# Optimization experiments

Measured on AMD Instinct MI355X. Metric: run time of the kernel, lower is better.

Reference implementation:

```python
import jax, jax.numpy as jnp
import numpy as np

# Dimensions / config (WorldModelConfig + PredictiveLayerConfig defaults)
S, N, L = 128, 256, 3          # n_sensory, n_hidden, n_layers
T, B = 100, 512                # timesteps, batch
TAU_MEM, TAU_PRED, DT = 20.0, 50.0, 1.0
NOISE_STD, ERROR_GAIN = 0.02, 0.5
DECAY_MEM = float(np.exp(-DT / TAU_MEM))
DECAY_PRED = float(np.exp(-DT / TAU_PRED))
ALPHA = DT / TAU_PRED          # precision EMA rate


def setup_inputs() -> dict:
    key = jax.random.key(0)
    ks = jax.random.split(key, 12)
    w = lambda k, a, b, s: jax.random.normal(k, (a, b), dtype=jnp.float32) * s
    return {
        'sensory_seq': jax.random.uniform(ks[0], (T, B, S), dtype=jnp.float32),
        'ff0': w(ks[1], S, N, 0.1 / S ** 0.5),
        'ff1': w(ks[2], N, N, 0.1 / N ** 0.5),
        'ff2': w(ks[3], N, N, 0.1 / N ** 0.5),
        'rec0': w(ks[4], N, N, 0.01),
        'rec1': w(ks[5], N, N, 0.01),
        'rec2': w(ks[6], N, N, 0.01),
        'pred0': w(ks[7], N, N, 0.1 / N ** 0.5),
        'pred1': w(ks[8], N, N, 0.1 / N ** 0.5),
        'p2r0': w(ks[9], N, N, 0.1 / N ** 0.5),
        'p2r1': w(ks[10], N, N, 0.1 / N ** 0.5),
    }


def _lif(v, inp, decay, noise):
    """LIF membrane update: leak + drive + noise, threshold=1.0, reset to 0."""
    v = decay * v + inp + noise
    s = (v >= 1.0).astype(v.dtype)
    return s, v * (1.0 - s)


def reference(sensory_seq, ff0, ff1, ff2, rec0, rec1, rec2, pred0, pred1, p2r0, p2r1):
    ffs = [ff0, ff1, ff2]
    recs = [rec0, rec1, rec2]
    preds = [pred0, pred1]
    p2rs = [p2r0, p2r1]
    mask = 1.0 - jnp.eye(N, dtype=sensory_seq.dtype)   # recurrent_mask
    base_key = jax.random.key(42)
    Bsz = sensory_seq.shape[1]

    init = (
        jnp.zeros((L, Bsz, N), jnp.float32),   # repr membrane
        jnp.zeros((2, Bsz, N), jnp.float32),   # pred membrane (layers 0,1)
        jnp.zeros((L, Bsz, N), jnp.float32),   # last spikes
        jnp.ones((L, Bsz, N), jnp.float32),    # precision
    )

    def step(carry, t):
        v, pv, last, prec = carry
        nks = jax.random.split(jax.random.fold_in(base_key, t), 5)
        new_v, new_pv, new_last, new_prec, errs = [], [], [], [], []
        for i in range(L):
            # top-down prediction from layer i+1's previous-step activity
            if i < L - 1:
                pred_in = last[i + 1] @ preds[i]
                pn = (NOISE_STD * 0.5) * jax.random.normal(nks[3 + i], (Bsz, N))
                psp, pvi = _lif(pv[i], pred_in, DECAY_PRED, pn)
                prediction = psp @ p2rs[i]
                new_pv.append(pvi)
            else:
                prediction = jnp.zeros((Bsz, N), jnp.float32)
            # bottom-up input: sensory for layer 0, lower layer's current spikes above
            inp_act = sensory_seq[t] if i == 0 else new_last[i - 1]
            input_repr = inp_act @ ffs[i]
            error = input_repr - prediction
            total = prediction + error * ERROR_GAIN * prec[i] + last[i] @ (recs[i] * mask)
            noi = NOISE_STD * jax.random.normal(nks[i], (Bsz, N))
            sp, vi = _lif(v[i], total, DECAY_MEM, noi)
            # precision EMA on inverse error variance
            ev = jnp.mean(error * error, axis=1, keepdims=True) + 1e-6
            pr = (1.0 - ALPHA) * prec[i] + ALPHA * (1.0 / ev)
            new_v.append(vi); new_last.append(sp); new_prec.append(pr); errs.append(error)
        carry = (jnp.stack(new_v), jnp.stack(new_pv), jnp.stack(new_last), jnp.stack(new_prec))
        return carry, jnp.stack(errs)   # [L, B, N] per step

    _, errors = jax.lax.scan(step, init, jnp.arange(T))
    return errors   # [T, L, B, N]
```

## Files before the change

### kernel.cpp

```cpp
#include <hip/hip_runtime.h>
#include <stdint.h>

#define TSTEPS 100
#define BATCH  512
#define NH     256
#define NS     128

__device__ __forceinline__ uint32_t rotl32(uint32_t x, int r) {
  return (x << r) | (x >> (32 - r));
}

__device__ __forceinline__ void tf2x32(uint32_t k0, uint32_t k1,
                                       uint32_t c0, uint32_t c1,
                                       uint32_t& o0, uint32_t& o1) {
  const uint32_t ks2 = k0 ^ k1 ^ 0x1BD11BDAu;
  uint32_t x0 = c0 + k0, x1 = c1 + k1;
#define TFR(r) { x0 += x1; x1 = rotl32(x1, r); x1 ^= x0; }
  TFR(13) TFR(15) TFR(26) TFR(6)
  x0 += k1;  x1 += ks2 + 1u;
  TFR(17) TFR(29) TFR(16) TFR(24)
  x0 += ks2; x1 += k0 + 2u;
  TFR(13) TFR(15) TFR(26) TFR(6)
  x0 += k0;  x1 += k1 + 3u;
  TFR(17) TFR(29) TFR(16) TFR(24)
  x0 += k1;  x1 += ks2 + 4u;
  TFR(13) TFR(15) TFR(26) TFR(6)
  x0 += ks2; x1 += k0 + 5u;
#undef TFR
  o0 = x0; o1 = x1;
}

__device__ __forceinline__ float xla_vf32_log(float a) {
  uint32_t bits = __float_as_uint(a);
  float e = __fadd_rn((float)((int)(bits >> 23) - 127), 1.0f);
  float x = __uint_as_float((bits & 0x007FFFFFu) | 0x3F000000u);
  const bool mask = x < 0.707106781186547524f;
  float tmp = mask ? x : 0.0f;
  x = __fsub_rn(x, 1.0f);
  e = mask ? __fsub_rn(e, 1.0f) : e;
  x = __fadd_rn(x, tmp);
  float z = __fmul_rn(x, x);
  float y = 7.0376836292e-2f;
  y = __fmaf_rn(y, x, -1.1514610310e-1f);
  y = __fmaf_rn(y, x, 1.1676998740e-1f);
  y = __fmaf_rn(y, x, -1.2420140846e-1f);
  y = __fmaf_rn(y, x, 1.4249322787e-1f);
  y = __fmaf_rn(y, x, -1.6668057665e-1f);
  y = __fmaf_rn(y, x, 2.0000714765e-1f);
  y = __fmaf_rn(y, x, -2.4999993993e-1f);
  y = __fmaf_rn(y, x, 3.3333331174e-1f);
  y = __fmul_rn(y, x);
  y = __fmul_rn(y, z);
  y = __fmaf_rn(e, -2.12194440e-4f, y);
  y = __fmaf_rn(-0.5f, z, y);
  x = __fadd_rn(x, y);
  x = __fmaf_rn(e, 0.693359375f, x);
  return x;
}

__device__ __forceinline__ float xla_sqrt2_erfinv(float u) {
  float nxx = -__fmul_rn(u, u);
  float w;
  if (fabsf(nxx) < 1e-4f) {
    w = -__fmul_rn(__fmaf_rn(-0.5f, nxx, 1.0f), nxx);
  } else {
    w = -xla_vf32_log(__fadd_rn(nxx, 1.0f));
  }
  float p;
  if (w < 5.0f) {
    float t = __fsub_rn(w, 2.5f);
    p = 2.81022636e-08f;
    p = __fmaf_rn(p, t, 3.43273939e-07f);
    p = __fmaf_rn(p, t, -3.5233877e-06f);
    p = __fmaf_rn(p, t, -4.39150654e-06f);
    p = __fmaf_rn(p, t, 0.00021858087f);
    p = __fmaf_rn(p, t, -0.00125372503f);
    p = __fmaf_rn(p, t, -0.00417768164f);
    p = __fmaf_rn(p, t, 0.246640727f);
    p = __fmaf_rn(p, t, 1.50140941f);
  } else {
    float t = __fsub_rn(__fsqrt_rn(w), 3.0f);
    p = -0.000200214257f;
    p = __fmaf_rn(p, t, 0.000100950558f);
    p = __fmaf_rn(p, t, 0.00134934322f);
    p = __fmaf_rn(p, t, -0.00367342844f);
    p = __fmaf_rn(p, t, 0.00573950773f);
    p = __fmaf_rn(p, t, -0.0076224613f);
    p = __fmaf_rn(p, t, 0.00943887047f);
    p = __fmaf_rn(p, t, 1.00167406f);
    p = __fmaf_rn(p, t, 2.83297682f);
  }
  return __fmul_rn((float)1.4142135623730951, __fmul_rn(p, u));
}

__device__ __forceinline__ float jax_normal(uint32_t k0, uint32_t k1, uint32_t j) {
  uint32_t o0, o1;
  tf2x32(k0, k1, 0u, j, o0, o1);
  const uint32_t bits = o0 ^ o1;
  float f = __fsub_rn(__uint_as_float((bits >> 9) | 0x3f800000u), 1.0f);
  const float LO = -0.99999994f;
  float u = __fmaf_rn(f, 2.0f, LO);
  u = fmaxf(LO, u);
  return xla_sqrt2_erfinv(u);
}

__global__ void pack_w(const float* __restrict__ src, float* __restrict__ dst,
                       int K, int zero_diag) {
  int tid = blockIdx.x * 256 + threadIdx.x;
  if (tid >= K * NH) return;
  int k = tid >> 8, n = tid & 255;
  float v = src[tid];
  if (zero_diag && k == n) v = 0.f;
  dst[(((k >> 2) * NH) + n) * 4 + (k & 3)] = v;
}

__global__ __launch_bounds__(256)
void gen_noise(float* __restrict__ NZ) {
  uint32_t idx = blockIdx.x * 256u + threadIdx.x;
  uint32_t j = idx & 131071u;
  uint32_t td = idx >> 17;
  uint32_t t = td / 5u, d = td - 5u * t;
  uint32_t fk0, fk1, k0, k1;
  tf2x32(0u, 42u, 0u, t, fk0, fk1);
  tf2x32(fk0, fk1, 0u, d, k0, k1);
  float z = jax_normal(k0, k1, j);
  float scale = (d >= 3u) ? 0.01f : 0.02f;
  NZ[idx] = __fmul_rn(scale, z);
}

__device__ __forceinline__ void dot1_seg(const float4* __restrict__ P0,
                                         const float* __restrict__ A0,
                                         int n, int k4b, int k4e, float& r0) {
  float a0 = r0;
  #pragma unroll 8
  for (int k4 = k4b; k4 < k4e; ++k4) {
    float4 w0 = P0[k4 * NH + n];
    float4 x0 = *reinterpret_cast<const float4*>(A0 + 4 * k4);
    a0 = __fmaf_rn(x0.x, w0.x, a0); a0 = __fmaf_rn(x0.y, w0.y, a0);
    a0 = __fmaf_rn(x0.z, w0.z, a0); a0 = __fmaf_rn(x0.w, w0.w, a0);
  }
  r0 = a0;
}

__device__ __forceinline__ void dot2_seg(const float4* __restrict__ P0,
                                         const float* __restrict__ A0,
                                         const float4* __restrict__ P1,
                                         const float* __restrict__ A1,
                                         int n, int k4b, int k4e,
                                         float& r0, float& r1) {
  float a0 = r0, a1 = r1;
  #pragma unroll 8
  for (int k4 = k4b; k4 < k4e; ++k4) {
    float4 w0 = P0[k4 * NH + n];
    float4 w1 = P1[k4 * NH + n];
    float4 x0 = *reinterpret_cast<const float4*>(A0 + 4 * k4);
    float4 x1 = *reinterpret_cast<const float4*>(A1 + 4 * k4);
    a0 = __fmaf_rn(x0.x, w0.x, a0); a0 = __fmaf_rn(x0.y, w0.y, a0);
    a0 = __fmaf_rn(x0.z, w0.z, a0); a0 = __fmaf_rn(x0.w, w0.w, a0);
    a1 = __fmaf_rn(x1.x, w1.x, a1); a1 = __fmaf_rn(x1.y, w1.y, a1);
    a1 = __fmaf_rn(x1.z, w1.z, a1); a1 = __fmaf_rn(x1.w, w1.w, a1);
  }
  r0 = a0; r1 = a1;
}

__global__ __launch_bounds__(512)
void wm_fast5(const float* __restrict__ sensory,
              const float4* __restrict__ pred0p, const float4* __restrict__ pred1p,
              const float4* __restrict__ p2r0p,  const float4* __restrict__ rec0p,
              const float4* __restrict__ ff0p,   const float4* __restrict__ p2r1p,
              const float4* __restrict__ ff1p,   const float4* __restrict__ rec1p,
              const float4* __restrict__ ff2p,   const float4* __restrict__ rec2p,
              const float* __restrict__ NZ,
              float* __restrict__ out) {
  const int tid = threadIdx.x;
  const int n = tid & 255;
  const int h = tid >> 8;
  const int b = blockIdx.x;

  __shared__ __align__(16) float last[2][3][NH];
  __shared__ __align__(16) float psp0[NH];
  __shared__ __align__(16) float psp1[NH];
  __shared__ __align__(16) float sens[NS];
  __shared__ __align__(16) float errsq[3][NH];
  __shared__ __align__(16) float xfer[NH];
  __shared__ float evsum[3];

  if (h == 0) {
    #pragma unroll
    for (int i = 0; i < 3; ++i) { last[0][i][n] = 0.f; last[1][i][n] = 0.f; }
  }

  float pv = 0.f, vA = 0.f, vB = 0.f;
  float prec0 = 1.f, prec1 = 1.f, prec2 = 1.f;
  const float DM = (float)0.951229424500714009;
  const float DP = (float)0.980198673306755250;

  __syncthreads();

  for (int t = 0; t < TSTEPS; ++t) {
    const int p = t & 1, q = p ^ 1;
    const size_t nb = ((size_t)t * 5 * BATCH + b) * NH + n;

    if (tid < NS) sens[tid] = sensory[((size_t)t * BATCH + b) * NS + tid];
    if (h == 0) {
      float acc = 0.f;
      dot1_seg(pred0p, last[p][1], n, 0, 64, acc);
      float pn = NZ[nb + (size_t)3 * BATCH * NH];
      pv = __fadd_rn(__fmaf_rn(DP, pv, acc), pn);
      bool s = (pv >= 1.0f);
      psp0[n] = s ? 1.f : 0.f;
      pv = s ? 0.f : pv;
    } else {
      float acc = 0.f;
      dot1_seg(pred1p, last[p][2], n, 0, 64, acc);
      float pn = NZ[nb + (size_t)4 * BATCH * NH];
      pv = __fadd_rn(__fmaf_rn(DP, pv, acc), pn);
      bool s = (pv >= 1.0f);
      psp1[n] = s ? 1.f : 0.f;
      pv = s ? 0.f : pv;
    }
    __syncthreads();

    float inp_b = 0.f, rc_b = 0.f;
    if (h == 0) {
      dot2_seg(ff0p, sens, rec0p, last[p][0], n, 0, 32, inp_b, rc_b);
      dot1_seg(rec0p, last[p][0], n, 32, 64, rc_b);
    } else {
      float pr = 0.f;
      dot1_seg(p2r0p, psp0, n, 0, 64, pr);
      xfer[n] = pr;
    }
    __syncthreads();
    if (h == 0) {
      float pr = xfer[n];
      float noi = NZ[nb];
      float err = __fsub_rn(inp_b, pr);
      out[(((size_t)t * 3 + 0) * BATCH + b) * NH + n] = err;
      errsq[0][n] = __fmul_rn(err, err);
      float m1  = __fmul_rn(err, 0.5f);
      float tot = __fadd_rn(__fmaf_rn(m1, prec0, pr), rc_b);
      vA = __fadd_rn(__fmaf_rn(DM, vA, tot), noi);
      bool s = (vA >= 1.0f);
      last[q][0][n] = s ? 1.f : 0.f;
      vA = s ? 0.f : vA;
    }
    __syncthreads();

    if (h == 0) {
      float inp = 0.f;
      dot1_seg(ff1p, last[q][0], n, 0, 64, inp);
      xfer[n] = inp;
    } else {
      float pr = 0.f, rc = 0.f;
      dot2_seg(p2r1p, psp1, rec1p, last[p][1], n, 0, 64, pr, rc);
      inp_b = pr; rc_b = rc;
    }
    __syncthreads();
    if (h == 1) {
      float pr = inp_b, rc = rc_b;
      float inp = xfer[n];
      float noi = NZ[nb + (size_t)1 * BATCH * NH];
      float err = __fsub_rn(inp, pr);
      out[(((size_t)t * 3 + 1) * BATCH + b) * NH + n] = err;
      errsq[1][n] = __fmul_rn(err, err);
      float m1  = __fmul_rn(err, 0.5f);
      float tot = __fadd_rn(__fmaf_rn(m1, prec1, pr), rc);
      vA = __fadd_rn(__fmaf_rn(DM, vA, tot), noi);
      bool s = (vA >= 1.0f);
      last[q][1][n] = s ? 1.f : 0.f;
      vA = s ? 0.f : vA;
    }
    __syncthreads();

    if (h == 0) {
      float inp = 0.f;
      dot1_seg(ff2p, last[q][1], n, 0, 64, inp);
      inp_b = inp;
    } else {
      float rc = 0.f;
      dot1_seg(rec2p, last[p][2], n, 0, 64, rc);
      xfer[n] = rc;
    }
    __syncthreads();
    if (h == 0) {
      float rc = xfer[n];
      float err = inp_b;
      float noi = NZ[nb + (size_t)2 * BATCH * NH];
      out[(((size_t)t * 3 + 2) * BATCH + b) * NH + n] = err;
      errsq[2][n] = __fmul_rn(err, err);
      float m1  = __fmul_rn(err, 0.5f);
      float tot = __fadd_rn(__fmaf_rn(m1, prec2, 0.0f), rc);
      vB = __fadd_rn(__fmaf_rn(DM, vB, tot), noi);
      bool s = (vB >= 1.0f);
      last[q][2][n] = s ? 1.f : 0.f;
      vB = s ? 0.f : vB;
    }
    __syncthreads();

    if (((tid & 63) == 0) && tid < 192) {
      const float4* s4 = reinterpret_cast<const float4*>(errsq[tid >> 6]);
      float acc = 0.f;
      #pragma unroll 16
      for (int k4 = 0; k4 < 64; ++k4) {
        float4 v = s4[k4];
        acc = __fadd_rn(acc, v.x); acc = __fadd_rn(acc, v.y);
        acc = __fadd_rn(acc, v.z); acc = __fadd_rn(acc, v.w);
      }
      evsum[tid >> 6] = acc;
    }
    __syncthreads();

    {
      float ev0 = __fadd_rn(__fmul_rn(evsum[0], 0.00390625f), 1e-6f);
      float ev1 = __fadd_rn(__fmul_rn(evsum[1], 0.00390625f), 1e-6f);
      float ev2 = __fadd_rn(__fmul_rn(evsum[2], 0.00390625f), 1e-6f);
      prec0 = __fmaf_rn(0.98f, prec0, __fmul_rn(0.02f, 1.0f / ev0));
      prec1 = __fmaf_rn(0.98f, prec1, __fmul_rn(0.02f, 1.0f / ev1));
      prec2 = __fmaf_rn(0.98f, prec2, __fmul_rn(0.02f, 1.0f / ev2));
    }
  }
}

__device__ __forceinline__ float dot_lds(const float* __restrict__ a,
                                         const float* __restrict__ W,
                                         int n, int K) {
  float acc = 0.f;
  #pragma unroll 8
  for (int k = 0; k < K; ++k)
    acc = __fmaf_rn(a[k], W[k * NH + n], acc);
  return acc;
}

__device__ __forceinline__ float dot_rec(const float* __restrict__ a,
                                         const float* __restrict__ W, int n) {
  float acc = 0.f;
  #pragma unroll 8
  for (int k = 0; k < NH; ++k) {
    float w = (k == n) ? 0.f : W[k * NH + n];
    acc = __fmaf_rn(a[k], w, acc);
  }
  return acc;
}

__global__ __launch_bounds__(NH)
void wm_kernel_mono(const float* __restrict__ sensory,
                    const float* __restrict__ ff0, const float* __restrict__ ff1,
                    const float* __restrict__ ff2,
                    const float* __restrict__ rec0, const float* __restrict__ rec1,
                    const float* __restrict__ rec2,
                    const float* __restrict__ pred0, const float* __restrict__ pred1,
                    const float* __restrict__ p2r0, const float* __restrict__ p2r1,
                    float* __restrict__ out) {
  const int b = blockIdx.x;
  const int n = threadIdx.x;

  __shared__ float last[2][3][NH];
  __shared__ float psp[NH];
  __shared__ float sens[NS];
  __shared__ float errsq[3][NH];
  __shared__ float evsum[3];
  __shared__ uint32_t keys[TSTEPS][5][2];

  if (n < TSTEPS) {
    uint32_t fk0, fk1;
    tf2x32(0u, 42u, 0u, (uint32_t)n, fk0, fk1);
    #pragma unroll
    for (int i = 0; i < 5; ++i) {
      uint32_t s0, s1;
      tf2x32(fk0, fk1, 0u, (uint32_t)i, s0, s1);
      keys[n][i][0] = s0; keys[n][i][1] = s1;
    }
  }
  for (int i = 0; i < 3; ++i) { last[0][i][n] = 0.f; last[1][i][n] = 0.f; }

  float v0 = 0.f, v1 = 0.f, v2 = 0.f, pv0 = 0.f, pv1 = 0.f;
  float prec0 = 1.f, prec1 = 1.f, prec2 = 1.f;
  const float DM = (float)0.951229424500714009;
  const float DP = (float)0.980198673306755250;
  const uint32_t j = (uint32_t)(b * NH + n);

  __syncthreads();

  for (int t = 0; t < TSTEPS; ++t) {
    const int p = t & 1, q = p ^ 1;

    if (n < NS) sens[n] = sensory[((size_t)t * BATCH + b) * NS + n];
    {
      float acc = dot_lds(last[p][1], pred0, n, NH);
      float pn = __fmul_rn(0.01f, jax_normal(keys[t][3][0], keys[t][3][1], j));
      pv0 = __fadd_rn(__fmaf_rn(DP, pv0, acc), pn);
      bool s = (pv0 >= 1.0f);
      psp[n] = s ? 1.f : 0.f;
      pv0 = s ? 0.f : pv0;
    }
    __syncthreads();

    {
      float pr  = dot_lds(psp, p2r0, n, NH);
      float inp = dot_lds(sens, ff0, n, NS);
      float rc  = dot_rec(last[p][0], rec0, n);
      float err = __fsub_rn(inp, pr);
      out[(((size_t)t * 3 + 0) * BATCH + b) * NH + n] = err;
      errsq[0][n] = __fmul_rn(err, err);
      float m1  = __fmul_rn(err, 0.5f);
      float tot = __fadd_rn(__fmaf_rn(m1, prec0, pr), rc);
      float noi = __fmul_rn(0.02f, jax_normal(keys[t][0][0], keys[t][0][1], j));
      v0 = __fadd_rn(__fmaf_rn(DM, v0, tot), noi);
      bool s = (v0 >= 1.0f);
      last[q][0][n] = s ? 1.f : 0.f;
      v0 = s ? 0.f : v0;
    }
    __syncthreads();

    {
      float acc = dot_lds(last[p][2], pred1, n, NH);
      float pn = __fmul_rn(0.01f, jax_normal(keys[t][4][0], keys[t][4][1], j));
      pv1 = __fadd_rn(__fmaf_rn(DP, pv1, acc), pn);
      bool s = (pv1 >= 1.0f);
      psp[n] = s ? 1.f : 0.f;
      pv1 = s ? 0.f : pv1;
    }
    __syncthreads();

    {
      float pr  = dot_lds(psp, p2r1, n, NH);
      float inp = dot_lds(last[q][0], ff1, n, NH);
      float rc  = dot_rec(last[p][1], rec1, n);
      float err = __fsub_rn(inp, pr);
      out[(((size_t)t * 3 + 1) * BATCH + b) * NH + n] = err;
      errsq[1][n] = __fmul_rn(err, err);
      float m1  = __fmul_rn(err, 0.5f);
      float tot = __fadd_rn(__fmaf_rn(m1, prec1, pr), rc);
      float noi = __fmul_rn(0.02f, jax_normal(keys[t][1][0], keys[t][1][1], j));
      v1 = __fadd_rn(__fmaf_rn(DM, v1, tot), noi);
      bool s = (v1 >= 1.0f);
      last[q][1][n] = s ? 1.f : 0.f;
      v1 = s ? 0.f : v1;
    }
    __syncthreads();

    {
      float inp = dot_lds(last[q][1], ff2, n, NH);
      float rc  = dot_rec(last[p][2], rec2, n);
      float err = inp;
      out[(((size_t)t * 3 + 2) * BATCH + b) * NH + n] = err;
      errsq[2][n] = __fmul_rn(err, err);
      float m1  = __fmul_rn(err, 0.5f);
      float tot = __fadd_rn(__fmaf_rn(m1, prec2, 0.0f), rc);
      float noi = __fmul_rn(0.02f, jax_normal(keys[t][2][0], keys[t][2][1], j));
      v2 = __fadd_rn(__fmaf_rn(DM, v2, tot), noi);
      bool s = (v2 >= 1.0f);
      last[q][2][n] = s ? 1.f : 0.f;
      v2 = s ? 0.f : v2;
    }
    __syncthreads();

    if (((n & 63) == 0) && n < 192) {
      const float* s = errsq[n >> 6];
      float acc = 0.f;
      #pragma unroll 32
      for (int k = 0; k < NH; ++k) acc = __fadd_rn(acc, s[k]);
      evsum[n >> 6] = acc;
    }
    __syncthreads();

    {
      float ev0 = __fadd_rn(__fmul_rn(evsum[0], 0.00390625f), 1e-6f);
      float ev1 = __fadd_rn(__fmul_rn(evsum[1], 0.00390625f), 1e-6f);
      float ev2 = __fadd_rn(__fmul_rn(evsum[2], 0.00390625f), 1e-6f);
      prec0 = __fmaf_rn(0.98f, prec0, __fmul_rn(0.02f, 1.0f / ev0));
      prec1 = __fmaf_rn(0.98f, prec1, __fmul_rn(0.02f, 1.0f / ev1));
      prec2 = __fmaf_rn(0.98f, prec2, __fmul_rn(0.02f, 1.0f / ev2));
    }
  }
}

extern "C" void kernel_launch(void* const* d_in, const int* in_sizes, int n_in,
                              void* d_out, int out_size, void* d_ws, size_t ws_size,
                              hipStream_t stream) {
  (void)in_sizes; (void)n_in; (void)out_size;
  const float* sensory = (const float*)d_in[0];
  const float* ff0  = (const float*)d_in[1];
  const float* ff1  = (const float*)d_in[2];
  const float* ff2  = (const float*)d_in[3];
  const float* rec0 = (const float*)d_in[4];
  const float* rec1 = (const float*)d_in[5];
  const float* rec2 = (const float*)d_in[6];
  const float* pred0 = (const float*)d_in[7];
  const float* pred1 = (const float*)d_in[8];
  const float* p2r0 = (const float*)d_in[9];
  const float* p2r1 = (const float*)d_in[10];
  float* out = (float*)d_out;

  const size_t OFF_PRED0 = 0, OFF_PRED1 = 65536, OFF_P2R0 = 131072,
               OFF_REC0 = 196608, OFF_FF0 = 262144, OFF_P2R1 = 294912,
               OFF_FF1 = 360448, OFF_REC1 = 425984, OFF_FF2 = 491520,
               OFF_REC2 = 557056, OFF_NZ = 655360;
  const size_t NZ_FLOATS = (size_t)TSTEPS * 5 * BATCH * NH;
  const size_t NEED = (OFF_NZ + NZ_FLOATS) * sizeof(float);

  if (ws_size >= NEED) {
    float* W = (float*)d_ws;
    pack_w<<<dim3(NH * NH / 256), dim3(256), 0, stream>>>(pred0, W + OFF_PRED0, NH, 0);
    pack_w<<<dim3(NH * NH / 256), dim3(256), 0, stream>>>(pred1, W + OFF_PRED1, NH, 0);
    pack_w<<<dim3(NH * NH / 256), dim3(256), 0, stream>>>(p2r0,  W + OFF_P2R0,  NH, 0);
    pack_w<<<dim3(NH * NH / 256), dim3(256), 0, stream>>>(rec0,  W + OFF_REC0,  NH, 1);
    pack_w<<<dim3(NS * NH / 256), dim3(256), 0, stream>>>(ff0,   W + OFF_FF0,   NS, 0);
    pack_w<<<dim3(NH * NH / 256), dim3(256), 0, stream>>>(p2r1,  W + OFF_P2R1,  NH, 0);
    pack_w<<<dim3(NH * NH / 256), dim3(256), 0, stream>>>(ff1,   W + OFF_FF1,   NH, 0);
    pack_w<<<dim3(NH * NH / 256), dim3(256), 0, stream>>>(rec1,  W + OFF_REC1,  NH, 1);
    pack_w<<<dim3(NH * NH / 256), dim3(256), 0, stream>>>(ff2,   W + OFF_FF2,   NH, 0);
    pack_w<<<dim3(NH * NH / 256), dim3(256), 0, stream>>>(rec2,  W + OFF_REC2,  NH, 1);
    gen_noise<<<dim3((unsigned)(NZ_FLOATS / 256)), dim3(256), 0, stream>>>(W + OFF_NZ);
    wm_fast5<<<dim3(BATCH), dim3(512), 0, stream>>>(
        sensory,
        (const float4*)(W + OFF_PRED0), (const float4*)(W + OFF_PRED1),
        (const float4*)(W + OFF_P2R0),  (const float4*)(W + OFF_REC0),
        (const float4*)(W + OFF_FF0),   (const float4*)(W + OFF_P2R1),
        (const float4*)(W + OFF_FF1),   (const float4*)(W + OFF_REC1),
        (const float4*)(W + OFF_FF2),   (const float4*)(W + OFF_REC2),
        W + OFF_NZ, out);
  } else {
    wm_kernel_mono<<<dim3(BATCH), dim3(NH), 0, stream>>>(
        sensory, ff0, ff1, ff2, rec0, rec1, rec2,
        pred0, pred1, p2r0, p2r1, out);
  }
}
```

Measured before the change: 4.691 ms.

## Process two batch rows per block to reuse each weight load twice

Each workgroup now handles two batch rows instead of one, so every float4 weight fetched from global/L2 feeds two accumulators. Shared buffers, membrane states and precision values are all duplicated per row, and the grid is halved to 256 blocks. This targets the weight-load bandwidth of the per-step matvecs. The cost is fewer blocks than the chip has CUs, more registers per thread, and a longer serial dependency chain per block, so parallelism drops.

```diff
diff --git a/kernel.cpp b/kernel.cpp
--- a/kernel.cpp
+++ b/kernel.cpp
@@ -128,43 +128,57 @@
   NZ[idx] = __fmul_rn(scale, z);
 }
 
-__device__ __forceinline__ void dot1_seg(const float4* __restrict__ P0,
-                                         const float* __restrict__ A0,
-                                         int n, int k4b, int k4e, float& r0) {
-  float a0 = r0;
-  #pragma unroll 8
-  for (int k4 = k4b; k4 < k4e; ++k4) {
-    float4 w0 = P0[k4 * NH + n];
-    float4 x0 = *reinterpret_cast<const float4*>(A0 + 4 * k4);
-    a0 = __fmaf_rn(x0.x, w0.x, a0); a0 = __fmaf_rn(x0.y, w0.y, a0);
-    a0 = __fmaf_rn(x0.z, w0.z, a0); a0 = __fmaf_rn(x0.w, w0.w, a0);
-  }
-  r0 = a0;
-}
-
-__device__ __forceinline__ void dot2_seg(const float4* __restrict__ P0,
-                                         const float* __restrict__ A0,
-                                         const float4* __restrict__ P1,
-                                         const float* __restrict__ A1,
-                                         int n, int k4b, int k4e,
-                                         float& r0, float& r1) {
+__device__ __forceinline__ void dotW2r(const float4* __restrict__ P,
+                                       const float* __restrict__ X0,
+                                       const float* __restrict__ X1,
+                                       int n, int k4b, int k4e,
+                                       float& r0, float& r1) {
   float a0 = r0, a1 = r1;
   #pragma unroll 8
   for (int k4 = k4b; k4 < k4e; ++k4) {
-    float4 w0 = P0[k4 * NH + n];
-    float4 w1 = P1[k4 * NH + n];
-    float4 x0 = *reinterpret_cast<const float4*>(A0 + 4 * k4);
-    float4 x1 = *reinterpret_cast<const float4*>(A1 + 4 * k4);
-    a0 = __fmaf_rn(x0.x, w0.x, a0); a0 = __fmaf_rn(x0.y, w0.y, a0);
-    a0 = __fmaf_rn(x0.z, w0.z, a0); a0 = __fmaf_rn(x0.w, w0.w, a0);
-    a1 = __fmaf_rn(x1.x, w1.x, a1); a1 = __fmaf_rn(x1.y, w1.y, a1);
-    a1 = __fmaf_rn(x1.z, w1.z, a1); a1 = __fmaf_rn(x1.w, w1.w, a1);
+    float4 w = P[k4 * NH + n];
+    float4 x0 = *(const float4*)(X0 + 4 * k4);
+    float4 x1 = *(const float4*)(X1 + 4 * k4);
+    a0 = __fmaf_rn(x0.x, w.x, a0); a1 = __fmaf_rn(x1.x, w.x, a1);
+    a0 = __fmaf_rn(x0.y, w.y, a0); a1 = __fmaf_rn(x1.y, w.y, a1);
+    a0 = __fmaf_rn(x0.z, w.z, a0); a1 = __fmaf_rn(x1.z, w.z, a1);
+    a0 = __fmaf_rn(x0.w, w.w, a0); a1 = __fmaf_rn(x1.w, w.w, a1);
   }
   r0 = a0; r1 = a1;
 }
 
+__device__ __forceinline__ void dot2W2r(const float4* __restrict__ PA,
+                                        const float* __restrict__ XA0,
+                                        const float* __restrict__ XA1,
+                                        const float4* __restrict__ PB,
+                                        const float* __restrict__ XB0,
+                                        const float* __restrict__ XB1,
+                                        int n, int k4b, int k4e,
+                                        float& rA0, float& rA1,
+                                        float& rB0, float& rB1) {
+  float a0 = rA0, a1 = rA1, b0 = rB0, b1 = rB1;
+  #pragma unroll 4
+  for (int k4 = k4b; k4 < k4e; ++k4) {
+    float4 wa = PA[k4 * NH + n];
+    float4 wb = PB[k4 * NH + n];
+    float4 xa0 = *(const float4*)(XA0 + 4 * k4);
+    float4 xa1 = *(const float4*)(XA1 + 4 * k4);
+    float4 xb0 = *(const float4*)(XB0 + 4 * k4);
+    float4 xb1 = *(const float4*)(XB1 + 4 * k4);
+    a0 = __fmaf_rn(xa0.x, wa.x, a0); a1 = __fmaf_rn(xa1.x, wa.x, a1);
+    b0 = __fmaf_rn(xb0.x, wb.x, b0); b1 = __fmaf_rn(xb1.x, wb.x, b1);
+    a0 = __fmaf_rn(xa0.y, wa.y, a0); a1 = __fmaf_rn(xa1.y, wa.y, a1);
+    b0 = __fmaf_rn(xb0.y, wb.y, b0); b1 = __fmaf_rn(xb1.y, wb.y, b1);
+    a0 = __fmaf_rn(xa0.z, wa.z, a0); a1 = __fmaf_rn(xa1.z, wa.z, a1);
+    b0 = __fmaf_rn(xb0.z, wb.z, b0); b1 = __fmaf_rn(xb1.z, wb.z, b1);
+    a0 = __fmaf_rn(xa0.w, wa.w, a0); a1 = __fmaf_rn(xa1.w, wa.w, a1);
+    b0 = __fmaf_rn(xb0.w, wb.w, b0); b1 = __fmaf_rn(xb1.w, wb.w, b1);
+  }
+  rA0 = a0; rA1 = a1; rB0 = b0; rB1 = b1;
+}
+
 __global__ __launch_bounds__(512)
-void wm_fast5(const float* __restrict__ sensory,
+void wm_fast7(const float* __restrict__ sensory,
               const float4* __restrict__ pred0p, const float4* __restrict__ pred1p,
               const float4* __restrict__ p2r0p,  const float4* __restrict__ rec0p,
               const float4* __restrict__ ff0p,   const float4* __restrict__ p2r1p,
@@ -175,23 +189,28 @@
   const int tid = threadIdx.x;
   const int n = tid & 255;
   const int h = tid >> 8;
-  const int b = blockIdx.x;
-
-  __shared__ __align__(16) float last[2][3][NH];
-  __shared__ __align__(16) float psp0[NH];
-  __shared__ __align__(16) float psp1[NH];
-  __shared__ __align__(16) float sens[NS];
-  __shared__ __align__(16) float errsq[3][NH];
-  __shared__ __align__(16) float xfer[NH];
-  __shared__ float evsum[3];
+  const int b0 = blockIdx.x * 2, b1 = b0 + 1;
+
+  __shared__ __align__(16) float last[2][3][2][NH];
+  __shared__ __align__(16) float psp0[2][NH];
+  __shared__ __align__(16) float psp1[2][NH];
+  __shared__ __align__(16) float sens[2][NS];
+  __shared__ __align__(16) float errsq[3][2][NH];
+  __shared__ __align__(16) float xfer[2][NH];
+  __shared__ float evsum[3][2];
 
   if (h == 0) {
     #pragma unroll
-    for (int i = 0; i < 3; ++i) { last[0][i][n] = 0.f; last[1][i][n] = 0.f; }
-  }
-
-  float pv = 0.f, vA = 0.f, vB = 0.f;
-  float prec0 = 1.f, prec1 = 1.f, prec2 = 1.f;
+    for (int i = 0; i < 3; ++i) {
+      last[0][i][0][n] = 0.f; last[0][i][1][n] = 0.f;
+      last[1][i][0][n] = 0.f; last[1][i][1][n] = 0.f;
+    }
+  }
+
+  float pvR0 = 0.f, pvR1 = 0.f;
+  float vX0 = 0.f, vX1 = 0.f;
+  float vY0 = 0.f, vY1 = 0.f;
+  float p0a = 1.f, p0b = 1.f, p1a = 1.f, p1b = 1.f, p2a = 1.f, p2b = 1.f;
   const float DM = (float)0.951229424500714009;
   const float DP = (float)0.980198673306755250;
 
@@ -199,106 +218,132 @@
 
   for (int t = 0; t < TSTEPS; ++t) {
     const int p = t & 1, q = p ^ 1;
-    const size_t nb = ((size_t)t * 5 * BATCH + b) * NH + n;
-
-    if (tid < NS) sens[tid] = sensory[((size_t)t * BATCH + b) * NS + tid];
+    const size_t t5 = (size_t)t * 5 * BATCH * NH;
+#define NZI(d, bb) (t5 + ((size_t)(d) * BATCH + (bb)) * NH + n)
+
+    if (tid < 2 * NS) {
+      int rr = tid >> 7, kk = tid & 127;
+      sens[rr][kk] = sensory[((size_t)t * BATCH + b0 + rr) * NS + kk];
+    }
     if (h == 0) {
-      float acc = 0.f;
-      dot1_seg(pred0p, last[p][1], n, 0, 64, acc);
-      float pn = NZ[nb + (size_t)3 * BATCH * NH];
-      pv = __fadd_rn(__fmaf_rn(DP, pv, acc), pn);
-      bool s = (pv >= 1.0f);
-      psp0[n] = s ? 1.f : 0.f;
-      pv = s ? 0.f : pv;
+      float a0 = 0.f, a1 = 0.f;
+      dotW2r(pred0p, last[p][1][0], last[p][1][1], n, 0, 64, a0, a1);
+      float pn0 = NZ[NZI(3, b0)], pn1 = NZ[NZI(3, b1)];
+      pvR0 = __fadd_rn(__fmaf_rn(DP, pvR0, a0), pn0);
+      bool s0 = (pvR0 >= 1.0f);
+      psp0[0][n] = s0 ? 1.f : 0.f;
+      pvR0 = s0 ? 0.f : pvR0;
+      pvR1 = __fadd_rn(__fmaf_rn(DP, pvR1, a1), pn1);
+      bool s1 = (pvR1 >= 1.0f);
+      psp0[1][n] = s1 ? 1.f : 0.f;
+      pvR1 = s1 ? 0.f : pvR1;
     } else {
-      float acc = 0.f;
-      dot1_seg(pred1p, last[p][2], n, 0, 64, acc);
-      float pn = NZ[nb + (size_t)4 * BATCH * NH];
-      pv = __fadd_rn(__fmaf_rn(DP, pv, acc), pn);
-      bool s = (pv >= 1.0f);
-      psp1[n] = s ? 1.f : 0.f;
-      pv = s ? 0.f : pv;
-    }
-    __syncthreads();
-
-    float inp_b = 0.f, rc_b = 0.f;
+      float a0 = 0.f, a1 = 0.f;
+      dotW2r(pred1p, last[p][2][0], last[p][2][1], n, 0, 64, a0, a1);
+      float pn0 = NZ[NZI(4, b0)], pn1 = NZ[NZI(4, b1)];
+      pvR0 = __fadd_rn(__fmaf_rn(DP, pvR0, a0), pn0);
+      bool s0 = (pvR0 >= 1.0f);
+      psp1[0][n] = s0 ? 1.f : 0.f;
+      pvR0 = s0 ? 0.f : pvR0;
+      pvR1 = __fadd_rn(__fmaf_rn(DP, pvR1, a1), pn1);
+      bool s1 = (pvR1 >= 1.0f);
+      psp1[1][n] = s1 ? 1.f : 0.f;
+      pvR1 = s1 ? 0.f : pvR1;
+    }
+    __syncthreads();
+
+    float sA0 = 0.f, sA1 = 0.f, sB0 = 0.f, sB1 = 0.f;
     if (h == 0) {
-      dot2_seg(ff0p, sens, rec0p, last[p][0], n, 0, 32, inp_b, rc_b);
-      dot1_seg(rec0p, last[p][0], n, 32, 64, rc_b);
+      dot2W2r(ff0p, sens[0], sens[1], rec0p, last[p][0][0], last[p][0][1],
+              n, 0, 32, sA0, sA1, sB0, sB1);
+      dotW2r(rec0p, last[p][0][0], last[p][0][1], n, 32, 64, sB0, sB1);
     } else {
-      float pr = 0.f;
-      dot1_seg(p2r0p, psp0, n, 0, 64, pr);
-      xfer[n] = pr;
+      float pr0 = 0.f, pr1 = 0.f;
+      dotW2r(p2r0p, psp0[0], psp0[1], n, 0, 64, pr0, pr1);
+      xfer[0][n] = pr0; xfer[1][n] = pr1;
     }
     __syncthreads();
     if (h == 0) {
-      float pr = xfer[n];
-      float noi = NZ[nb];
-      float err = __fsub_rn(inp_b, pr);
-      out[(((size_t)t * 3 + 0) * BATCH + b) * NH + n] = err;
-      errsq[0][n] = __fmul_rn(err, err);
-      float m1  = __fmul_rn(err, 0.5f);
-      float tot = __fadd_rn(__fmaf_rn(m1, prec0, pr), rc_b);
-      vA = __fadd_rn(__fmaf_rn(DM, vA, tot), noi);
-      bool s = (vA >= 1.0f);
-      last[q][0][n] = s ? 1.f : 0.f;
-      vA = s ? 0.f : vA;
+      float pr0 = xfer[0][n], pr1 = xfer[1][n];
+      float noi0 = NZ[NZI(0, b0)], noi1 = NZ[NZI(0, b1)];
+      float e0 = __fsub_rn(sA0, pr0), e1 = __fsub_rn(sA1, pr1);
+      out[(((size_t)t * 3 + 0) * BATCH + b0) * NH + n] = e0;
+      out[(((size_t)t * 3 + 0) * BATCH + b1) * NH + n] = e1;
+      errsq[0][0][n] = __fmul_rn(e0, e0);
+      errsq[0][1][n] = __fmul_rn(e1, e1);
+      float m0 = __fmul_rn(e0, 0.5f), m1 = __fmul_rn(e1, 0.5f);
+      float t0 = __fadd_rn(__fmaf_rn(m0, p0a, pr0), sB0);
+      float t1 = __fadd_rn(__fmaf_rn(m1, p0b, pr1), sB1);
+      vX0 = __fadd_rn(__fmaf_rn(DM, vX0, t0), noi0);
+      vX1 = __fadd_rn(__fmaf_rn(DM, vX1, t1), noi1);
+      bool s0 = (vX0 >= 1.0f), s1 = (vX1 >= 1.0f);
+      last[q][0][0][n] = s0 ? 1.f : 0.f;
+      last[q][0][1][n] = s1 ? 1.f : 0.f;
+      vX0 = s0 ? 0.f : vX0; vX1 = s1 ? 0.f : vX1;
     }
     __syncthreads();
 
     if (h == 0) {
-      float inp = 0.f;
-      dot1_seg(ff1p, last[q][0], n, 0, 64, inp);
-      xfer[n] = inp;
+      float i0 = 0.f, i1 = 0.f;
+      dotW2r(ff1p, last[q][0][0], last[q][0][1], n, 0, 64, i0, i1);
+      xfer[0][n] = i0; xfer[1][n] = i1;
     } else {
-      float pr = 0.f, rc = 0.f;
-      dot2_seg(p2r1p, psp1, rec1p, last[p][1], n, 0, 64, pr, rc);
-      inp_b = pr; rc_b = rc;
+      dot2W2r(p2r1p, psp1[0], psp1[1], rec1p, last[p][1][0], last[p][1][1],
+              n, 0, 64, sA0, sA1, sB0, sB1);
     }
     __syncthreads();
     if (h == 1) {
-      float pr = inp_b, rc = rc_b;
-      float inp = xfer[n];
-      float noi = NZ[nb + (size_t)1 * BATCH * NH];
-      float err = __fsub_rn(inp, pr);
-      out[(((size_t)t * 3 + 1) * BATCH + b) * NH + n] = err;
-      errsq[1][n] = __fmul_rn(err, err);
-      float m1  = __fmul_rn(err, 0.5f);
-      float tot = __fadd_rn(__fmaf_rn(m1, prec1, pr), rc);
-      vA = __fadd_rn(__fmaf_rn(DM, vA, tot), noi);
-      bool s = (vA >= 1.0f);
-      last[q][1][n] = s ? 1.f : 0.f;
-      vA = s ? 0.f : vA;
+      float i0 = xfer[0][n], i1 = xfer[1][n];
+      float noi0 = NZ[NZI(1, b0)], noi1 = NZ[NZI(1, b1)];
+      float e0 = __fsub_rn(i0, sA0), e1 = __fsub_rn(i1, sA1);
+      out[(((size_t)t * 3 + 1) * BATCH + b0) * NH + n] = e0;
+      out[(((size_t)t * 3 + 1) * BATCH + b1) * NH + n] = e1;
+      errsq[1][0][n] = __fmul_rn(e0, e0);
+      errsq[1][1][n] = __fmul_rn(e1, e1);
+      float m0 = __fmul_rn(e0, 0.5f), m1 = __fmul_rn(e1, 0.5f);
+      float t0 = __fadd_rn(__fmaf_rn(m0, p1a, sA0), sB0);
+      float t1 = __fadd_rn(__fmaf_rn(m1, p1b, sA1), sB1);
+      vX0 = __fadd_rn(__fmaf_rn(DM, vX0, t0), noi0);
+      vX1 = __fadd_rn(__fmaf_rn(DM, vX1, t1), noi1);
+      bool s0 = (vX0 >= 1.0f), s1 = (vX1 >= 1.0f);
+      last[q][1][0][n] = s0 ? 1.f : 0.f;
+      last[q][1][1][n] = s1 ? 1.f : 0.f;
+      vX0 = s0 ? 0.f : vX0; vX1 = s1 ? 0.f : vX1;
     }
     __syncthreads();
 
     if (h == 0) {
-      float inp = 0.f;
-      dot1_seg(ff2p, last[q][1], n, 0, 64, inp);
-      inp_b = inp;
+      sA0 = 0.f; sA1 = 0.f;
+      dotW2r(ff2p, last[q][1][0], last[q][1][1], n, 0, 64, sA0, sA1);
     } else {
-      float rc = 0.f;
-      dot1_seg(rec2p, last[p][2], n, 0, 64, rc);
-      xfer[n] = rc;
+      float rc0 = 0.f, rc1 = 0.f;
+      dotW2r(rec2p, last[p][2][0], last[p][2][1], n, 0, 64, rc0, rc1);
+      xfer[0][n] = rc0; xfer[1][n] = rc1;
     }
     __syncthreads();
     if (h == 0) {
-      float rc = xfer[n];
-      float err = inp_b;
-      float noi = NZ[nb + (size_t)2 * BATCH * NH];
-      out[(((size_t)t * 3 + 2) * BATCH + b) * NH + n] = err;
-      errsq[2][n] = __fmul_rn(err, err);
-      float m1  = __fmul_rn(err, 0.5f);
-      float tot = __fadd_rn(__fmaf_rn(m1, prec2, 0.0f), rc);
-      vB = __fadd_rn(__fmaf_rn(DM, vB, tot), noi);
-      bool s = (vB >= 1.0f);
-      last[q][2][n] = s ? 1.f : 0.f;
-      vB = s ? 0.f : vB;
-    }
-    __syncthreads();
-
-    if (((tid & 63) == 0) && tid < 192) {
-      const float4* s4 = reinterpret_cast<const float4*>(errsq[tid >> 6]);
+      float rc0 = xfer[0][n], rc1 = xfer[1][n];
+      float noi0 = NZ[NZI(2, b0)], noi1 = NZ[NZI(2, b1)];
+      float e0 = sA0, e1 = sA1;
+      out[(((size_t)t * 3 + 2) * BATCH + b0) * NH + n] = e0;
+      out[(((size_t)t * 3 + 2) * BATCH + b1) * NH + n] = e1;
+      errsq[2][0][n] = __fmul_rn(e0, e0);
+      errsq[2][1][n] = __fmul_rn(e1, e1);
+      float m0 = __fmul_rn(e0, 0.5f), m1 = __fmul_rn(e1, 0.5f);
+      float t0 = __fadd_rn(__fmaf_rn(m0, p2a, 0.0f), rc0);
+      float t1 = __fadd_rn(__fmaf_rn(m1, p2b, 0.0f), rc1);
+      vY0 = __fadd_rn(__fmaf_rn(DM, vY0, t0), noi0);
+      vY1 = __fadd_rn(__fmaf_rn(DM, vY1, t1), noi1);
+      bool s0 = (vY0 >= 1.0f), s1 = (vY1 >= 1.0f);
+      last[q][2][0][n] = s0 ? 1.f : 0.f;
+      last[q][2][1][n] = s1 ? 1.f : 0.f;
+      vY0 = s0 ? 0.f : vY0; vY1 = s1 ? 0.f : vY1;
+    }
+    __syncthreads();
+
+    if (tid < 6) {
+      const int l = tid >> 1, rr = tid & 1;
+      const float4* s4 = (const float4*)errsq[l][rr];
       float acc = 0.f;
       #pragma unroll 16
       for (int k4 = 0; k4 < 64; ++k4) {
@@ -306,18 +351,26 @@
         acc = __fadd_rn(acc, v.x); acc = __fadd_rn(acc, v.y);
         acc = __fadd_rn(acc, v.z); acc = __fadd_rn(acc, v.w);
       }
-      evsum[tid >> 6] = acc;
-    }
-    __syncthreads();
-
-    {
-      float ev0 = __fadd_rn(__fmul_rn(evsum[0], 0.00390625f), 1e-6f);
-      float ev1 = __fadd_rn(__fmul_rn(evsum[1], 0.00390625f), 1e-6f);
-      float ev2 = __fadd_rn(__fmul_rn(evsum[2], 0.00390625f), 1e-6f);
-      prec0 = __fmaf_rn(0.98f, prec0, __fmul_rn(0.02f, 1.0f / ev0));
-      prec1 = __fmaf_rn(0.98f, prec1, __fmul_rn(0.02f, 1.0f / ev1));
-      prec2 = __fmaf_rn(0.98f, prec2, __fmul_rn(0.02f, 1.0f / ev2));
-    }
+      evsum[l][rr] = acc;
+    }
+    __syncthreads();
+
+    {
+      float ev;
+      ev = __fadd_rn(__fmul_rn(evsum[0][0], 0.00390625f), 1e-6f);
+      p0a = __fmaf_rn(0.98f, p0a, __fmul_rn(0.02f, 1.0f / ev));
+      ev = __fadd_rn(__fmul_rn(evsum[0][1], 0.00390625f), 1e-6f);
+      p0b = __fmaf_rn(0.98f, p0b, __fmul_rn(0.02f, 1.0f / ev));
+      ev = __fadd_rn(__fmul_rn(evsum[1][0], 0.00390625f), 1e-6f);
+      p1a = __fmaf_rn(0.98f, p1a, __fmul_rn(0.02f, 1.0f / ev));
+      ev = __fadd_rn(__fmul_rn(evsum[1][1], 0.00390625f), 1e-6f);
+      p1b = __fmaf_rn(0.98f, p1b, __fmul_rn(0.02f, 1.0f / ev));
+      ev = __fadd_rn(__fmul_rn(evsum[2][0], 0.00390625f), 1e-6f);
+      p2a = __fmaf_rn(0.98f, p2a, __fmul_rn(0.02f, 1.0f / ev));
+      ev = __fadd_rn(__fmul_rn(evsum[2][1], 0.00390625f), 1e-6f);
+      p2b = __fmaf_rn(0.98f, p2b, __fmul_rn(0.02f, 1.0f / ev));
+    }
+#undef NZI
   }
 }
 
@@ -512,7 +565,7 @@
     pack_w<<<dim3(NH * NH / 256), dim3(256), 0, stream>>>(ff2,   W + OFF_FF2,   NH, 0);
     pack_w<<<dim3(NH * NH / 256), dim3(256), 0, stream>>>(rec2,  W + OFF_REC2,  NH, 1);
     gen_noise<<<dim3((unsigned)(NZ_FLOATS / 256)), dim3(256), 0, stream>>>(W + OFF_NZ);
-    wm_fast5<<<dim3(BATCH), dim3(512), 0, stream>>>(
+    wm_fast7<<<dim3(BATCH / 2), dim3(512), 0, stream>>>(
         sensory,
         (const float4*)(W + OFF_PRED0), (const float4*)(W + OFF_PRED1),
         (const float4*)(W + OFF_P2R0),  (const float4*)(W + OFF_REC0),
```

Result: faster. 4.525 ms (-3.5%).
